# Kernel tuning notes

Measured on AMD Instinct MI355X. Metric: run time of the kernel, lower is better.

## Reference

```python
import jax, jax.numpy as jnp
import numpy as np

N = 100000
METADATA = [128, 64, 32, 16]   # channels per degree l = 0..3
N_INV = METADATA[0]            # 128 invariant (l=0) channels
NUM_CH = sum(METADATA)         # 240 total channels
DIM = sum(m * (2 * l + 1) for l, m in enumerate(METADATA))  # 592 columns
EPS = 1e-5


def make_rep_layout():
    # column -> channel index, channels ordered by degree
    segs, off = [], 0
    for l, m in enumerate(METADATA):
        segs.append(np.repeat(np.arange(m) + off, 2 * l + 1))
        off += m
    return jnp.asarray(np.concatenate(segs), dtype=jnp.int64)


def setup_inputs() -> dict:
    key = jax.random.key(0)
    ks = jax.random.split(key, 5)
    ten = jax.random.normal(ks[0], (N, DIM), dtype=jnp.float32)
    w1 = jax.random.normal(ks[1], (NUM_CH, N_INV), dtype=jnp.float32) / np.sqrt(NUM_CH)
    w2 = jax.random.normal(ks[2], (N_INV, N_INV), dtype=jnp.float32) / np.sqrt(N_INV)
    w3 = jax.random.normal(ks[3], (N_INV, N_INV), dtype=jnp.float32) / np.sqrt(N_INV)
    return {
        "ten": ten,
        "rep_layout": make_rep_layout(),
        "w1": w1,
        "g1": jnp.ones((N_INV,), jnp.float32),
        "beta1": jnp.zeros((N_INV,), jnp.float32),
        "w2": w2,
        "b2": jnp.zeros((N_INV,), jnp.float32),
        "g2": jnp.ones((N_INV,), jnp.float32),
        "beta2": jnp.zeros((N_INV,), jnp.float32),
        "w3": w3,
        "b3": jnp.zeros((N_INV,), jnp.float32),
    }


def _layernorm(x, g, b):
    mu = jnp.mean(x, axis=-1, keepdims=True)
    var = jnp.var(x, axis=-1, keepdims=True)
    return (x - mu) * jax.lax.rsqrt(var + EPS) * g + b


def reference(ten, rep_layout, w1, g1, beta1, w2, b2, g2, beta2, w3, b3):
    # --- EvNorm1d (n_invariant_channels > 0 branch) ---
    x10 = ten[:, :N_INV]                         # [N, 128] invariant part
    eq = ten[:, N_INV:]                          # [N, 464] equivariant part
    seg = rep_layout[N_INV:] - N_INV             # column -> eq channel (0..111)
    n_eq = NUM_CH - N_INV                        # 112 equivariant channels
    # segment sum of squares over columns, keyed by channel
    sumsq = jax.ops.segment_sum((eq * eq).T, seg, num_segments=n_eq).T  # [N, 112]
    divisor = jnp.sqrt(sumsq + 1.0)
    x11 = divisor - 1.0
    x1 = jnp.concatenate([x10, x11], axis=1)     # [N, 240]
    x2 = eq / divisor[:, seg]                    # broadcast-divide via gather
    # --- MLP on invariant content ---
    h = x1 @ w1                                  # Linear(240->128, no bias)
    h = _layernorm(h, g1, beta1)
    h = h @ w2 + b2
    h = jax.nn.silu(h)
    h = _layernorm(h, g2, beta2)
    h = h @ w3 + b3
    return jnp.concatenate([h, x2], axis=-1)     # [N, 592]
```

## Files before the change

kernel.cpp:

```cpp
#include <hip/hip_runtime.h>

#define NROWS   100000
#define DIM     592
#define NINV    128
#define NEQ     112
#define NCH     240
#define ROWS    32
#define BLK     256
#define HPAD    129

typedef float f32x4 __attribute__((ext_vector_type(4)));

__global__ __launch_bounds__(BLK, 2)
void evmlp_kernel(const float* __restrict__ ten,
                  const float* __restrict__ w1,
                  const float* __restrict__ g1,
                  const float* __restrict__ be1,
                  const float* __restrict__ w2,
                  const float* __restrict__ b2,
                  const float* __restrict__ g2,
                  const float* __restrict__ be2,
                  const float* __restrict__ w3,
                  const float* __restrict__ b3,
                  float* __restrict__ out)
{
    __shared__ __align__(16) float sXT[NCH * ROWS];
    __shared__ __align__(16) float sH [ROWS * HPAD];

    const int t  = threadIdx.x;
    const int r0 = blockIdx.x * ROWS;

    for (int i = t; i < ROWS * NINV; i += BLK) {
        int r = i >> 7, k = i & 127;
        sXT[k * ROWS + r] = ten[(size_t)(r0 + r) * DIM + k];
    }
    for (int i = t; i < ROWS * NEQ; i += BLK) {
        int r = i / NEQ, c = i - r * NEQ;
        int base, nc;
        if (c < 64)      { base = 3 * c;              nc = 3; }
        else if (c < 96) { base = 192 + 5 * (c - 64); nc = 5; }
        else             { base = 352 + 7 * (c - 96); nc = 7; }
        const float* p = ten + (size_t)(r0 + r) * DIM + NINV + base;
        float vals[7];
        float ss = 1.0f;
        for (int j = 0; j < nc; ++j) { float v = p[j]; vals[j] = v; ss += v * v; }
        float dv  = sqrtf(ss);
        float inv = 1.0f / dv;
        sXT[(NINV + c) * ROWS + r] = dv - 1.0f;
        float* po = out + (size_t)(r0 + r) * DIM + NINV + base;
        for (int j = 0; j < nc; ++j) po[j] = vals[j] * inv;
    }
    __syncthreads();

    const int cgrp = t & 31;
    const int rgrp = t >> 5;
    const int c0 = cgrp << 2;
    const int rr = rgrp << 2;

    float acc[4][4];

    #pragma unroll
    for (int i = 0; i < 4; ++i)
        #pragma unroll
        for (int j = 0; j < 4; ++j) acc[i][j] = 0.f;
    {
        const float* wp = w1 + c0;
        #pragma unroll 8
        for (int k = 0; k < NCH; ++k) {
            f32x4 wv = *(const f32x4*)(wp + k * NINV);
            f32x4 xv = *(const f32x4*)(sXT + k * ROWS + rr);
            #pragma unroll
            for (int i = 0; i < 4; ++i)
                #pragma unroll
                for (int j = 0; j < 4; ++j)
                    acc[i][j] += xv[i] * wv[j];
        }
    }
    #pragma unroll
    for (int i = 0; i < 4; ++i)
        #pragma unroll
        for (int j = 0; j < 4; ++j)
            sH[(rr + i) * HPAD + c0 + j] = acc[i][j];
    __syncthreads();

    {
        const int row = t >> 3, j = t & 7;
        float vals[16];
        float s = 0.f, ss = 0.f;
        #pragma unroll
        for (int i = 0; i < 16; ++i) {
            float v = sH[row * HPAD + (i * 8 + j)];
            vals[i] = v; s += v; ss += v * v;
        }
        #pragma unroll
        for (int off = 1; off < 8; off <<= 1) {
            s  += __shfl_xor(s,  off);
            ss += __shfl_xor(ss, off);
        }
        float mu   = s * (1.f / 128.f);
        float var  = ss * (1.f / 128.f) - mu * mu;
        float rstd = rsqrtf(var + 1e-5f);
        #pragma unroll
        for (int i = 0; i < 16; ++i) {
            int c = i * 8 + j;
            sXT[c * ROWS + row] = (vals[i] - mu) * rstd * g1[c] + be1[c];
        }
    }
    __syncthreads();

    #pragma unroll
    for (int i = 0; i < 4; ++i)
        #pragma unroll
        for (int j = 0; j < 4; ++j) acc[i][j] = 0.f;
    {
        const float* wp = w2 + c0;
        #pragma unroll 8
        for (int k = 0; k < 128; ++k) {
            f32x4 wv = *(const f32x4*)(wp + k * 128);
            f32x4 xv = *(const f32x4*)(sXT + k * ROWS + rr);
            #pragma unroll
            for (int i = 0; i < 4; ++i)
                #pragma unroll
                for (int j = 0; j < 4; ++j)
                    acc[i][j] += xv[i] * wv[j];
        }
    }
    {
        f32x4 bv = *(const f32x4*)(b2 + c0);
        #pragma unroll
        for (int i = 0; i < 4; ++i)
            #pragma unroll
            for (int j = 0; j < 4; ++j) {
                float v = acc[i][j] + bv[j];
                v = v / (1.f + __expf(-v));
                sH[(rr + i) * HPAD + c0 + j] = v;
            }
    }
    __syncthreads();

    {
        const int row = t >> 3, j = t & 7;
        float vals[16];
        float s = 0.f, ss = 0.f;
        #pragma unroll
        for (int i = 0; i < 16; ++i) {
            float v = sH[row * HPAD + (i * 8 + j)];
            vals[i] = v; s += v; ss += v * v;
        }
        #pragma unroll
        for (int off = 1; off < 8; off <<= 1) {
            s  += __shfl_xor(s,  off);
            ss += __shfl_xor(ss, off);
        }
        float mu   = s * (1.f / 128.f);
        float var  = ss * (1.f / 128.f) - mu * mu;
        float rstd = rsqrtf(var + 1e-5f);
        #pragma unroll
        for (int i = 0; i < 16; ++i) {
            int c = i * 8 + j;
            sXT[c * ROWS + row] = (vals[i] - mu) * rstd * g2[c] + be2[c];
        }
    }
    __syncthreads();

    #pragma unroll
    for (int i = 0; i < 4; ++i)
        #pragma unroll
        for (int j = 0; j < 4; ++j) acc[i][j] = 0.f;
    {
        const float* wp = w3 + c0;
        #pragma unroll 8
        for (int k = 0; k < 128; ++k) {
            f32x4 wv = *(const f32x4*)(wp + k * 128);
            f32x4 xv = *(const f32x4*)(sXT + k * ROWS + rr);
            #pragma unroll
            for (int i = 0; i < 4; ++i)
                #pragma unroll
                for (int j = 0; j < 4; ++j)
                    acc[i][j] += xv[i] * wv[j];
        }
    }
    {
        f32x4 bv = *(const f32x4*)(b3 + c0);
        #pragma unroll
        for (int i = 0; i < 4; ++i) {
            f32x4 o;
            o.x = acc[i][0] + bv.x;
            o.y = acc[i][1] + bv.y;
            o.z = acc[i][2] + bv.z;
            o.w = acc[i][3] + bv.w;
            *(f32x4*)(out + (size_t)(r0 + rr + i) * DIM + c0) = o;
        }
    }
}

extern "C" void kernel_launch(void* const* d_in, const int* in_sizes, int n_in,
                              void* d_out, int out_size, void* d_ws, size_t ws_size,
                              hipStream_t stream) {
    const float* ten = (const float*)d_in[0];
    const float* w1  = (const float*)d_in[2];
    const float* g1  = (const float*)d_in[3];
    const float* be1 = (const float*)d_in[4];
    const float* w2  = (const float*)d_in[5];
    const float* b2  = (const float*)d_in[6];
    const float* g2  = (const float*)d_in[7];
    const float* be2 = (const float*)d_in[8];
    const float* w3  = (const float*)d_in[9];
    const float* b3  = (const float*)d_in[10];
    float* out = (float*)d_out;

    dim3 grid(NROWS / ROWS);
    dim3 block(BLK);
    evmlp_kernel<<<grid, block, 0, stream>>>(ten, w1, g1, be1, w2, b2, g2, be2, w3, b3, out);
}
```

Before: 704.7 us.

## Use 64-row tiles with 8x8 register blocking and split-K GEMMs over swizzled LDS

Doubles the row tile to 64 and gives each thread an 8x8 output block. The K dimension is split across two thread halves whose partial sums are exchanged through LDS, and the layernorm and activation are fused into that reduction step. LDS now uses a row-major layout with an XOR swizzle and vectorized f32x4 loads of the invariant input, aiming for more arithmetic per weight load and fewer bank conflicts. The 64-float accumulator raises register pressure and may lower occupancy, and a tail block with clamped reads is added for the row count that no longer divides evenly.

```diff
diff --git a/kernel.cpp b/kernel.cpp
--- a/kernel.cpp
+++ b/kernel.cpp
@@ -5,11 +5,16 @@
 #define NINV    128
 #define NEQ     112
 #define NCH     240
-#define ROWS    32
+#define ROWS    64
 #define BLK     256
-#define HPAD    129
+#define HOFF    8192
+#define GRID    ((NROWS + ROWS - 1) / ROWS)
 
 typedef float f32x4 __attribute__((ext_vector_type(4)));
+
+__device__ __forceinline__ int swz(int q, int r) {
+    return (q & ~3) | ((q ^ (r >> 3)) & 3);
+}
 
 __global__ __launch_bounds__(BLK, 2)
 void evmlp_kernel(const float* __restrict__ ten,
@@ -24,172 +29,206 @@
                   const float* __restrict__ b3,
                   float* __restrict__ out)
 {
-    __shared__ __align__(16) float sXT[NCH * ROWS];
-    __shared__ __align__(16) float sH [ROWS * HPAD];
+    __shared__ __align__(16) float lds[16384];
 
     const int t  = threadIdx.x;
     const int r0 = blockIdx.x * ROWS;
 
-    for (int i = t; i < ROWS * NINV; i += BLK) {
-        int r = i >> 7, k = i & 127;
-        sXT[k * ROWS + r] = ten[(size_t)(r0 + r) * DIM + k];
-    }
+    #pragma unroll
+    for (int it = 0; it < 8; ++it) {
+        int i = t + it * BLK;
+        int r = i >> 5, q = i & 31;
+        int rd = r0 + r; if (rd >= NROWS) rd = NROWS - 1;
+        f32x4 v = *(const f32x4*)(ten + (size_t)rd * DIM + (q << 2));
+        *(f32x4*)(lds + r * NCH + (swz(q, r) << 2)) = v;
+    }
+
     for (int i = t; i < ROWS * NEQ; i += BLK) {
         int r = i / NEQ, c = i - r * NEQ;
+        int rd = r0 + r; const bool valid = rd < NROWS; if (!valid) rd = NROWS - 1;
         int base, nc;
         if (c < 64)      { base = 3 * c;              nc = 3; }
         else if (c < 96) { base = 192 + 5 * (c - 64); nc = 5; }
         else             { base = 352 + 7 * (c - 96); nc = 7; }
-        const float* p = ten + (size_t)(r0 + r) * DIM + NINV + base;
-        float vals[7];
-        float ss = 1.0f;
-        for (int j = 0; j < nc; ++j) { float v = p[j]; vals[j] = v; ss += v * v; }
-        float dv  = sqrtf(ss);
-        float inv = 1.0f / dv;
-        sXT[(NINV + c) * ROWS + r] = dv - 1.0f;
-        float* po = out + (size_t)(r0 + r) * DIM + NINV + base;
-        for (int j = 0; j < nc; ++j) po[j] = vals[j] * inv;
-    }
-    __syncthreads();
-
-    const int cgrp = t & 31;
-    const int rgrp = t >> 5;
-    const int c0 = cgrp << 2;
-    const int rr = rgrp << 2;
-
-    float acc[4][4];
-
-    #pragma unroll
-    for (int i = 0; i < 4; ++i)
-        #pragma unroll
-        for (int j = 0; j < 4; ++j) acc[i][j] = 0.f;
+        const float* p = ten + (size_t)rd * DIM + NINV + base;
+        float vals[7]; float ssq = 1.0f;
+        for (int j = 0; j < nc; ++j) { float v = p[j]; vals[j] = v; ssq += v * v; }
+        float dv = sqrtf(ssq), inv = 1.0f / dv;
+        int k = NINV + c;
+        lds[r * NCH + (swz(k >> 2, r) << 2) + (k & 3)] = dv - 1.0f;
+        if (valid) {
+            float* po = out + (size_t)rd * DIM + NINV + base;
+            for (int j = 0; j < nc; ++j) po[j] = vals[j] * inv;
+        }
+    }
+    __syncthreads();
+
+    const int cgrp = t & 15;
+    const int rgrp = (t >> 4) & 7;
+    const int kg   = t >> 7;
+    const int rr   = rgrp << 3;
+    const int par  = rgrp & 1;
+    const int qA   = 2 * cgrp + par;
+    const int qB   = 2 * cgrp + 1 - par;
+    const int colA = qA << 2;
+    const int colB = qB << 2;
+
+    float acc[8][8];
+
+    auto zero_acc = [&]() {
+        #pragma unroll
+        for (int i = 0; i < 8; ++i)
+            #pragma unroll
+            for (int j = 0; j < 8; ++j) acc[i][j] = 0.f;
+    };
+
+    auto run_gemm = [&](const float* __restrict__ w, const float* xb, int xstride,
+                        int kbase, int kn) {
+        #pragma unroll 2
+        for (int kc = 0; kc < kn; kc += 4) {
+            const int k0 = kbase + kc;
+            const int pg = swz(k0 >> 2, rr) << 2;
+            f32x4 xv[8];
+            #pragma unroll
+            for (int i = 0; i < 8; ++i)
+                xv[i] = *(const f32x4*)(xb + (rr + i) * xstride + pg);
+            #pragma unroll
+            for (int kk = 0; kk < 4; ++kk) {
+                f32x4 wa = *(const f32x4*)(w + (size_t)(k0 + kk) * NINV + colA);
+                f32x4 wb = *(const f32x4*)(w + (size_t)(k0 + kk) * NINV + colB);
+                #pragma unroll
+                for (int i = 0; i < 8; ++i) {
+                    const float x = xv[i][kk];
+                    acc[i][0] += x * wa[0]; acc[i][1] += x * wa[1];
+                    acc[i][2] += x * wa[2]; acc[i][3] += x * wa[3];
+                    acc[i][4] += x * wb[0]; acc[i][5] += x * wb[1];
+                    acc[i][6] += x * wb[2]; acc[i][7] += x * wb[3];
+                }
+            }
+        }
+    };
+
+    auto put_partial = [&]() {
+        const int io = 4 * (1 - kg);
+        #pragma unroll
+        for (int i2 = 0; i2 < 4; ++i2) {
+            const int r = rr + io + i2;
+            f32x4 a = { acc[io+i2][0], acc[io+i2][1], acc[io+i2][2], acc[io+i2][3] };
+            f32x4 b = { acc[io+i2][4], acc[io+i2][5], acc[io+i2][6], acc[io+i2][7] };
+            *(f32x4*)(lds + r * NINV + (swz(qA, r) << 2)) = a;
+            *(f32x4*)(lds + r * NINV + (swz(qB, r) << 2)) = b;
+        }
+    };
+
+    zero_acc();
+    run_gemm(w1, lds, NCH, kg * 120, 120);
+    __syncthreads();
+    put_partial();
+    __syncthreads();
     {
-        const float* wp = w1 + c0;
-        #pragma unroll 8
-        for (int k = 0; k < NCH; ++k) {
-            f32x4 wv = *(const f32x4*)(wp + k * NINV);
-            f32x4 xv = *(const f32x4*)(sXT + k * ROWS + rr);
-            #pragma unroll
-            for (int i = 0; i < 4; ++i)
-                #pragma unroll
-                for (int j = 0; j < 4; ++j)
-                    acc[i][j] += xv[i] * wv[j];
-        }
-    }
-    #pragma unroll
-    for (int i = 0; i < 4; ++i)
-        #pragma unroll
-        for (int j = 0; j < 4; ++j)
-            sH[(rr + i) * HPAD + c0 + j] = acc[i][j];
-    __syncthreads();
-
+        const int io = 4 * kg;
+        f32x4 ga = *(const f32x4*)(g1 + colA), gb = *(const f32x4*)(g1 + colB);
+        f32x4 ba = *(const f32x4*)(be1 + colA), bb = *(const f32x4*)(be1 + colB);
+        #pragma unroll
+        for (int i2 = 0; i2 < 4; ++i2) {
+            const int r = rr + io + i2;
+            f32x4 pa = *(const f32x4*)(lds + r * NINV + (swz(qA, r) << 2));
+            f32x4 pb = *(const f32x4*)(lds + r * NINV + (swz(qB, r) << 2));
+            float v[8];
+            #pragma unroll
+            for (int j = 0; j < 4; ++j) {
+                v[j]     = acc[io+i2][j]     + pa[j];
+                v[4 + j] = acc[io+i2][4 + j] + pb[j];
+            }
+            float s = 0.f, s2 = 0.f;
+            #pragma unroll
+            for (int j = 0; j < 8; ++j) { s += v[j]; s2 += v[j] * v[j]; }
+            #pragma unroll
+            for (int off = 1; off < 16; off <<= 1) {
+                s  += __shfl_xor(s,  off);
+                s2 += __shfl_xor(s2, off);
+            }
+            const float mu   = s * (1.f / 128.f);
+            const float rstd = rsqrtf(s2 * (1.f / 128.f) - mu * mu + 1e-5f);
+            f32x4 ha, hb;
+            #pragma unroll
+            for (int j = 0; j < 4; ++j) {
+                ha[j] = (v[j]     - mu) * rstd * ga[j] + ba[j];
+                hb[j] = (v[4 + j] - mu) * rstd * gb[j] + bb[j];
+            }
+            *(f32x4*)(lds + HOFF + r * NINV + (swz(qA, r) << 2)) = ha;
+            *(f32x4*)(lds + HOFF + r * NINV + (swz(qB, r) << 2)) = hb;
+        }
+    }
+    __syncthreads();
+
+    zero_acc();
+    run_gemm(w2, lds + HOFF, NINV, kg * 64, 64);
+    put_partial();
+    __syncthreads();
     {
-        const int row = t >> 3, j = t & 7;
-        float vals[16];
-        float s = 0.f, ss = 0.f;
-        #pragma unroll
-        for (int i = 0; i < 16; ++i) {
-            float v = sH[row * HPAD + (i * 8 + j)];
-            vals[i] = v; s += v; ss += v * v;
-        }
-        #pragma unroll
-        for (int off = 1; off < 8; off <<= 1) {
-            s  += __shfl_xor(s,  off);
-            ss += __shfl_xor(ss, off);
-        }
-        float mu   = s * (1.f / 128.f);
-        float var  = ss * (1.f / 128.f) - mu * mu;
-        float rstd = rsqrtf(var + 1e-5f);
-        #pragma unroll
-        for (int i = 0; i < 16; ++i) {
-            int c = i * 8 + j;
-            sXT[c * ROWS + row] = (vals[i] - mu) * rstd * g1[c] + be1[c];
-        }
-    }
-    __syncthreads();
-
-    #pragma unroll
-    for (int i = 0; i < 4; ++i)
-        #pragma unroll
-        for (int j = 0; j < 4; ++j) acc[i][j] = 0.f;
+        const int io = 4 * kg;
+        f32x4 ga  = *(const f32x4*)(g2 + colA),  gb  = *(const f32x4*)(g2 + colB);
+        f32x4 ba  = *(const f32x4*)(be2 + colA), bb  = *(const f32x4*)(be2 + colB);
+        f32x4 b2a = *(const f32x4*)(b2 + colA),  b2b = *(const f32x4*)(b2 + colB);
+        #pragma unroll
+        for (int i2 = 0; i2 < 4; ++i2) {
+            const int r = rr + io + i2;
+            f32x4 pa = *(const f32x4*)(lds + r * NINV + (swz(qA, r) << 2));
+            f32x4 pb = *(const f32x4*)(lds + r * NINV + (swz(qB, r) << 2));
+            float v[8];
+            #pragma unroll
+            for (int j = 0; j < 4; ++j) {
+                float x0 = acc[io+i2][j]     + pa[j] + b2a[j];
+                float x1 = acc[io+i2][4 + j] + pb[j] + b2b[j];
+                v[j]     = x0 / (1.f + __expf(-x0));
+                v[4 + j] = x1 / (1.f + __expf(-x1));
+            }
+            float s = 0.f, s2 = 0.f;
+            #pragma unroll
+            for (int j = 0; j < 8; ++j) { s += v[j]; s2 += v[j] * v[j]; }
+            #pragma unroll
+            for (int off = 1; off < 16; off <<= 1) {
+                s  += __shfl_xor(s,  off);
+                s2 += __shfl_xor(s2, off);
+            }
+            const float mu   = s * (1.f / 128.f);
+            const float rstd = rsqrtf(s2 * (1.f / 128.f) - mu * mu + 1e-5f);
+            f32x4 ha, hb;
+            #pragma unroll
+            for (int j = 0; j < 4; ++j) {
+                ha[j] = (v[j]     - mu) * rstd * ga[j] + ba[j];
+                hb[j] = (v[4 + j] - mu) * rstd * gb[j] + bb[j];
+            }
+            *(f32x4*)(lds + HOFF + r * NINV + (swz(qA, r) << 2)) = ha;
+            *(f32x4*)(lds + HOFF + r * NINV + (swz(qB, r) << 2)) = hb;
+        }
+    }
+    __syncthreads();
+
+    zero_acc();
+    run_gemm(w3, lds + HOFF, NINV, kg * 64, 64);
+    put_partial();
+    __syncthreads();
     {
-        const float* wp = w2 + c0;
-        #pragma unroll 8
-        for (int k = 0; k < 128; ++k) {
-            f32x4 wv = *(const f32x4*)(wp + k * 128);
-            f32x4 xv = *(const f32x4*)(sXT + k * ROWS + rr);
-            #pragma unroll
-            for (int i = 0; i < 4; ++i)
-                #pragma unroll
-                for (int j = 0; j < 4; ++j)
-                    acc[i][j] += xv[i] * wv[j];
-        }
-    }
-    {
-        f32x4 bv = *(const f32x4*)(b2 + c0);
-        #pragma unroll
-        for (int i = 0; i < 4; ++i)
-            #pragma unroll
-            for (int j = 0; j < 4; ++j) {
-                float v = acc[i][j] + bv[j];
-                v = v / (1.f + __expf(-v));
-                sH[(rr + i) * HPAD + c0 + j] = v;
-            }
-    }
-    __syncthreads();
-
-    {
-        const int row = t >> 3, j = t & 7;
-        float vals[16];
-        float s = 0.f, ss = 0.f;
-        #pragma unroll
-        for (int i = 0; i < 16; ++i) {
-            float v = sH[row * HPAD + (i * 8 + j)];
-            vals[i] = v; s += v; ss += v * v;
-        }
-        #pragma unroll
-        for (int off = 1; off < 8; off <<= 1) {
-            s  += __shfl_xor(s,  off);
-            ss += __shfl_xor(ss, off);
-        }
-        float mu   = s * (1.f / 128.f);
-        float var  = ss * (1.f / 128.f) - mu * mu;
-        float rstd = rsqrtf(var + 1e-5f);
-        #pragma unroll
-        for (int i = 0; i < 16; ++i) {
-            int c = i * 8 + j;
-            sXT[c * ROWS + row] = (vals[i] - mu) * rstd * g2[c] + be2[c];
-        }
-    }
-    __syncthreads();
-
-    #pragma unroll
-    for (int i = 0; i < 4; ++i)
-        #pragma unroll
-        for (int j = 0; j < 4; ++j) acc[i][j] = 0.f;
-    {
-        const float* wp = w3 + c0;
-        #pragma unroll 8
-        for (int k = 0; k < 128; ++k) {
-            f32x4 wv = *(const f32x4*)(wp + k * 128);
-            f32x4 xv = *(const f32x4*)(sXT + k * ROWS + rr);
-            #pragma unroll
-            for (int i = 0; i < 4; ++i)
-                #pragma unroll
-                for (int j = 0; j < 4; ++j)
-                    acc[i][j] += xv[i] * wv[j];
-        }
-    }
-    {
-        f32x4 bv = *(const f32x4*)(b3 + c0);
-        #pragma unroll
-        for (int i = 0; i < 4; ++i) {
-            f32x4 o;
-            o.x = acc[i][0] + bv.x;
-            o.y = acc[i][1] + bv.y;
-            o.z = acc[i][2] + bv.z;
-            o.w = acc[i][3] + bv.w;
-            *(f32x4*)(out + (size_t)(r0 + rr + i) * DIM + c0) = o;
+        const int io = 4 * kg;
+        f32x4 b3a = *(const f32x4*)(b3 + colA), b3b = *(const f32x4*)(b3 + colB);
+        #pragma unroll
+        for (int i2 = 0; i2 < 4; ++i2) {
+            const int r  = rr + io + i2;
+            const int rd = r0 + r;
+            f32x4 pa = *(const f32x4*)(lds + r * NINV + (swz(qA, r) << 2));
+            f32x4 pb = *(const f32x4*)(lds + r * NINV + (swz(qB, r) << 2));
+            f32x4 oa, ob;
+            #pragma unroll
+            for (int j = 0; j < 4; ++j) {
+                oa[j] = acc[io+i2][j]     + pa[j] + b3a[j];
+                ob[j] = acc[io+i2][4 + j] + pb[j] + b3b[j];
+            }
+            if (rd < NROWS) {
+                *(f32x4*)(out + (size_t)rd * DIM + colA) = oa;
+                *(f32x4*)(out + (size_t)rd * DIM + colB) = ob;
+            }
         }
     }
 }
@@ -209,7 +248,7 @@
     const float* b3  = (const float*)d_in[10];
     float* out = (float*)d_out;
 
-    dim3 grid(NROWS / ROWS);
+    dim3 grid(GRID);
     dim3 block(BLK);
     evmlp_kernel<<<grid, block, 0, stream>>>(ten, w1, g1, be1, w2, b2, g2, be2, w3, b3, out);
 }
```

Measured after the change: 828.6 us. 1.18x slower.
